# Optimization experiments

Hardware: AMD Instinct MI355X
Metric: run time of the kernel (lower is better)

## Reference

```python
import jax, jax.numpy as jnp
import numpy as np


def setup_inputs() -> dict:
    key = jax.random.key(0)
    k1, k2 = jax.random.split(key)
    N, D, n_bags, per_bag = 8192, 512, 64, 128
    features = jax.random.normal(k1, (N, D), dtype=jnp.float32)
    # sorted bag indicator: 64 bags x 128 instances each
    batch = jnp.repeat(jnp.arange(n_bags, dtype=jnp.int32), per_bag)
    W = jax.random.normal(k2, (D, D), dtype=jnp.float32) * np.float32(1.0 / np.sqrt(D))
    b = jnp.zeros((D,), dtype=jnp.float32)
    return {"features": features, "W": W, "b": b, "batch": batch, "n_topk": 16, "n_bags": n_bags}


def reference(features, W, b, batch, n_topk, n_bags):
    N = features.shape[0]
    # F.normalize(dim=1): x / max(||x||, eps)
    norm = jnp.sqrt(jnp.sum(features * features, axis=1, keepdims=True))
    nf = features / jnp.maximum(norm, 1e-12)
    corr = nf @ nf.T  # [N, N] cosine-similarity map
    same_bag = batch[:, None] == batch[None, :]
    adj = jnp.where(same_bag, corr, 0.0)
    # scatter-zero the (N - n_topk) smallest per row == keep n_topk largest per row
    _, top_idx = jax.lax.top_k(adj, n_topk)  # [N, n_topk]
    keep = jnp.zeros((N, N), dtype=bool).at[jnp.arange(N)[:, None], top_idx].set(True)
    adj = jnp.where(keep, adj, 0.0)
    # dense_to_sparse()[0] keeps only indices -> unit edge weights for GCNConv.
    # GCNConv (gcn_norm, add_self_loops=True): A_hat = binarized adjacency with diag forced to 1.
    eye = jnp.eye(N, dtype=bool)
    A = jnp.where(eye, 1.0, (adj != 0).astype(features.dtype))  # [N, N]
    deg = jnp.sum(A, axis=0)  # degree scattered on target (col) index in PyG
    dis = jax.lax.rsqrt(deg)  # deg >= 1 thanks to self loops
    xw = features @ W  # [N, D]
    # out[col] = d[col]^-1/2 * sum_row A[row,col] * d[row]^-1/2 * xw[row]
    gcn_out = dis[:, None] * (A.T @ (dis[:, None] * xw)) + b
    # one-hot^T @ features == per-bag segment sum
    agg = jax.ops.segment_sum(gcn_out, batch, num_segments=n_bags)  # [n_bags, D]
    return agg, adj
```

## Files before the change

### kernel.cpp

```cpp
#include <hip/hip_runtime.h>
#include <hip/hip_bf16.h>

#define N 8192
#define D 512
#define NBAGS 64
#define PER_BAG 128
#define TOPK 16

typedef float vfloat4 __attribute__((ext_vector_type(4)));

#define WS_INVN   0
#define WS_KIDX   32768
#define WS_KCNT   557056
#define WS_DEG    589824
#define WS_FW     622592

__global__ void norm_kernel(const float* __restrict__ feat,
                            float* __restrict__ invn,
                            int* __restrict__ deg) {
    int t = threadIdx.x;
    if (blockIdx.x < 32) deg[blockIdx.x * 256 + t] = 0;
    int lane = t & 63, w = t >> 6;
    int r = blockIdx.x * 4 + w;
    const float4* fr = (const float4*)(feat + (size_t)r * D);
    float4 a = fr[lane];
    float4 bq = fr[lane + 64];
    float ss = a.x * a.x + a.y * a.y + a.z * a.z + a.w * a.w
             + bq.x * bq.x + bq.y * bq.y + bq.z * bq.z + bq.w * bq.w;
    #pragma unroll
    for (int off = 32; off > 0; off >>= 1) ss += __shfl_down(ss, off);
    if (lane == 0) invn[r] = 1.0f / fmaxf(sqrtf(ss), 1e-12f);
}

__global__ __launch_bounds__(256, 4) void simtopk_kernel(
        const float* __restrict__ feat,
        const float* __restrict__ invn,
        float* __restrict__ adjOut,
        int* __restrict__ keptIdx,
        int* __restrict__ keptCnt,
        int* __restrict__ deg) {
    int rg = blockIdx.x;
    int bag = blockIdx.y;
    int t = threadIdx.x;
    __shared__ float colT[32][132];
    __shared__ float rowT[32][12];
    int bagBase = bag * PER_BAG;
    int rowBase = bagBase + rg * 8;
    int tx = t & 31;
    int ty = t >> 5;
    float4 acc = make_float4(0.f, 0.f, 0.f, 0.f);

    int kk = t & 31;
    int sub = t >> 5;
    int winHalf = bag >> 5;
    int jw = (bag & 31) >> 3;
    int winLo = (bag & 31) * 32, winHi = winLo + 32;
    vfloat4 zf4 = {0.f, 0.f, 0.f, 0.f};

    for (int it = 0; it < 16; ++it) {
        int k0 = it * 32;
        __syncthreads();
        #pragma unroll
        for (int c0 = 0; c0 < 16; ++c0) {
            int c = sub * 16 + c0;
            colT[kk][c] = feat[(size_t)(bagBase + c) * D + k0 + kk];
        }
        rowT[kk][sub] = feat[(size_t)(rowBase + sub) * D + k0 + kk];
        __syncthreads();
        {
            int zr = it >> 1, half = it & 1;
            vfloat4* rowp = (vfloat4*)(adjOut + (size_t)(rowBase + zr) * N)
                            + half * 1024;
            bool hasWin = (half == winHalf);
            #pragma unroll
            for (int j = 0; j < 4; ++j) {
                int f = t + 256 * j;
                if (hasWin && j == jw) {
                    if (f < winLo || f >= winHi)
                        __builtin_nontemporal_store(zf4, &rowp[f]);
                } else {
                    __builtin_nontemporal_store(zf4, &rowp[f]);
                }
            }
        }
        #pragma unroll
        for (int k = 0; k < 32; ++k) {
            float4 cv = *(const float4*)&colT[k][4 * tx];
            float rv = rowT[k][ty];
            acc.x += rv * cv.x; acc.y += rv * cv.y;
            acc.z += rv * cv.z; acc.w += rv * cv.w;
        }
    }
    float ic0 = invn[bagBase + 4 * tx];
    float ic1 = invn[bagBase + 4 * tx + 1];
    float ic2 = invn[bagBase + 4 * tx + 2];
    float ic3 = invn[bagBase + 4 * tx + 3];
    float ir = invn[rowBase + ty];
    acc.x *= ir * ic0; acc.y *= ir * ic1;
    acc.z *= ir * ic2; acc.w *= ir * ic3;

    {
        int r = rowBase + ty;
        float o0 = acc.x, o1 = acc.y, o2 = acc.z, o3 = acc.w;
        float w0 = o0, w1 = o1, w2 = o2, w3 = o3;
        int pm = 0, cnt = 0;
        #pragma unroll 1
        for (int itk = 0; itk < TOPK; ++itk) {
            float bv = w0; int bj = 0;
            if (w1 > bv) { bv = w1; bj = 1; }
            if (w2 > bv) { bv = w2; bj = 2; }
            if (w3 > bv) { bv = w3; bj = 3; }
            int bi = 4 * tx + bj;
            #pragma unroll
            for (int s = 1; s < 32; s <<= 1) {
                float ov = __shfl_xor(bv, s);
                int oi = __shfl_xor(bi, s);
                if (ov > bv || (ov == bv && oi < bi)) { bv = ov; bi = oi; }
            }
            if (bv <= 0.0f) break;
            if (tx == 0) keptIdx[(size_t)r * TOPK + cnt] = bi;
            cnt++;
            if ((bi >> 2) == tx) {
                pm |= 1 << (bi & 3);
                int q = bi & 3;
                if (q == 0) w0 = -1e30f;
                else if (q == 1) w1 = -1e30f;
                else if (q == 2) w2 = -1e30f;
                else w3 = -1e30f;
            }
        }
        if (tx == 0) keptCnt[r] = cnt;
        float4 ov4 = make_float4((pm & 1) ? o0 : 0.0f,
                                 (pm & 2) ? o1 : 0.0f,
                                 (pm & 4) ? o2 : 0.0f,
                                 (pm & 8) ? o3 : 0.0f);
        *(float4*)(adjOut + (size_t)r * N + bagBase + 4 * tx) = ov4;
        if (pm & 1) atomicAdd(&deg[bagBase + 4 * tx], 1);
        if (pm & 2) atomicAdd(&deg[bagBase + 4 * tx + 1], 1);
        if (pm & 4) atomicAdd(&deg[bagBase + 4 * tx + 2], 1);
        if (pm & 8) atomicAdd(&deg[bagBase + 4 * tx + 3], 1);
        int selfCol = rg * 8 + ty;
        if (tx == (selfCol >> 2) && !((pm >> (selfCol & 3)) & 1))
            atomicAdd(&deg[bagBase + selfCol], 1);
    }
}

__global__ void wfw_kernel(const float* __restrict__ feat,
                           const int* __restrict__ keptIdx,
                           const int* __restrict__ keptCnt,
                           const int* __restrict__ deg,
                           float* __restrict__ FW) {
    int bag = blockIdx.x;
    int chunk = blockIdx.y;
    int t = threadIdx.x;
    __shared__ float wsh[PER_BAG];
    int bagBase = bag * PER_BAG;
    {
        int r = bagBase + t;
        int cnt = keptCnt[r];
        float sum = 0.0f;
        bool selfin = false;
        for (int k = 0; k < cnt; ++k) {
            int c = keptIdx[(size_t)r * TOPK + k];
            if (c == t) selfin = true;
            sum += rsqrtf((float)deg[bagBase + c]);
        }
        float disr = rsqrtf((float)deg[r]);
        if (!selfin) sum += disr;
        wsh[t] = disr * sum;
    }
    __syncthreads();
    int d = chunk * 128 + t;
    float acc = 0.0f;
    #pragma unroll 8
    for (int r = 0; r < PER_BAG; ++r)
        acc += wsh[r] * feat[(size_t)(bagBase + r) * D + d];
    FW[bag * D + d] = acc;
}

__global__ void agg_kernel(const float* __restrict__ FW,
                           const float* __restrict__ Wm,
                           const float* __restrict__ b,
                           float* __restrict__ aggOut) {
    int bag = blockIdx.x;
    int chunk = blockIdx.y;
    int t = threadIdx.x;
    __shared__ float fws[D];
    fws[t] = FW[bag * D + t];
    fws[256 + t] = FW[bag * D + 256 + t];
    __syncthreads();
    int d = chunk * 256 + t;
    float acc = 0.0f;
    #pragma unroll 8
    for (int k = 0; k < D; ++k)
        acc += fws[k] * Wm[(size_t)k * D + d];
    aggOut[bag * D + d] = acc + 128.0f * b[d];
}

extern "C" void kernel_launch(void* const* d_in, const int* in_sizes, int n_in,
                              void* d_out, int out_size, void* d_ws, size_t ws_size,
                              hipStream_t stream) {
    const float* feat = (const float*)d_in[0];
    const float* Wm   = (const float*)d_in[1];
    const float* b    = (const float*)d_in[2];

    char* ws = (char*)d_ws;
    float* invn   = (float*)(ws + WS_INVN);
    int* keptIdx  = (int*)(ws + WS_KIDX);
    int* keptCnt  = (int*)(ws + WS_KCNT);
    int* deg      = (int*)(ws + WS_DEG);
    float* FW     = (float*)(ws + WS_FW);

    float* aggOut = (float*)d_out;
    float* adjOut = (float*)d_out + NBAGS * D;

    norm_kernel<<<N / 4, 256, 0, stream>>>(feat, invn, deg);
    simtopk_kernel<<<dim3(16, NBAGS), 256, 0, stream>>>(feat, invn, adjOut,
                                                        keptIdx, keptCnt, deg);
    wfw_kernel<<<dim3(NBAGS, 4), PER_BAG, 0, stream>>>(feat, keptIdx, keptCnt,
                                                       deg, FW);
    agg_kernel<<<dim3(NBAGS, 2), 256, 0, stream>>>(FW, Wm, b, aggOut);
}
```

Measured before the change: 344.3 us.

## Move adjacency zero-fill from simtopk kernel into norm kernel

```diff
diff --git a/kernel.cpp b/kernel.cpp
--- a/kernel.cpp
+++ b/kernel.cpp
@@ -15,13 +15,15 @@
 #define WS_DEG    589824
 #define WS_FW     622592
 
-__global__ void norm_kernel(const float* __restrict__ feat,
-                            float* __restrict__ invn,
-                            int* __restrict__ deg) {
-    int t = threadIdx.x;
-    if (blockIdx.x < 32) deg[blockIdx.x * 256 + t] = 0;
+__global__ void norm_fill_kernel(const float* __restrict__ feat,
+                                 float* __restrict__ invn,
+                                 int* __restrict__ deg,
+                                 float* __restrict__ adjOut) {
+    int t = threadIdx.x;
+    int b = blockIdx.x;
+    if (b < 32) deg[b * 256 + t] = 0;
     int lane = t & 63, w = t >> 6;
-    int r = blockIdx.x * 4 + w;
+    int r = b * 4 + w;
     const float4* fr = (const float4*)(feat + (size_t)r * D);
     float4 a = fr[lane];
     float4 bq = fr[lane + 64];
@@ -30,6 +32,11 @@
     #pragma unroll
     for (int off = 32; off > 0; off >>= 1) ss += __shfl_down(ss, off);
     if (lane == 0) invn[r] = 1.0f / fmaxf(sqrtf(ss), 1e-12f);
+    vfloat4 z = {0.f, 0.f, 0.f, 0.f};
+    vfloat4* base = (vfloat4*)(adjOut + (size_t)b * 4 * N);
+    #pragma unroll
+    for (int j = 0; j < 32; ++j)
+        __builtin_nontemporal_store(z, &base[t + 256 * j]);
 }
 
 __global__ __launch_bounds__(256, 4) void simtopk_kernel(
@@ -52,10 +59,6 @@
 
     int kk = t & 31;
     int sub = t >> 5;
-    int winHalf = bag >> 5;
-    int jw = (bag & 31) >> 3;
-    int winLo = (bag & 31) * 32, winHi = winLo + 32;
-    vfloat4 zf4 = {0.f, 0.f, 0.f, 0.f};
 
     for (int it = 0; it < 16; ++it) {
         int k0 = it * 32;
@@ -67,22 +70,6 @@
         }
         rowT[kk][sub] = feat[(size_t)(rowBase + sub) * D + k0 + kk];
         __syncthreads();
-        {
-            int zr = it >> 1, half = it & 1;
-            vfloat4* rowp = (vfloat4*)(adjOut + (size_t)(rowBase + zr) * N)
-                            + half * 1024;
-            bool hasWin = (half == winHalf);
-            #pragma unroll
-            for (int j = 0; j < 4; ++j) {
-                int f = t + 256 * j;
-                if (hasWin && j == jw) {
-                    if (f < winLo || f >= winHi)
-                        __builtin_nontemporal_store(zf4, &rowp[f]);
-                } else {
-                    __builtin_nontemporal_store(zf4, &rowp[f]);
-                }
-            }
-        }
         #pragma unroll
         for (int k = 0; k < 32; ++k) {
             float4 cv = *(const float4*)&colT[k][4 * tx];
@@ -214,7 +201,7 @@
     float* aggOut = (float*)d_out;
     float* adjOut = (float*)d_out + NBAGS * D;
 
-    norm_kernel<<<N / 4, 256, 0, stream>>>(feat, invn, deg);
+    norm_fill_kernel<<<N / 4, 256, 0, stream>>>(feat, invn, deg, adjOut);
     simtopk_kernel<<<dim3(16, NBAGS), 256, 0, stream>>>(feat, invn, adjOut,
                                                         keptIdx, keptCnt, deg);
     wfw_kernel<<<dim3(NBAGS, 4), PER_BAG, 0, stream>>>(feat, keptIdx, keptCnt,
```

New measurement: 387.9 us. 1.13x slower.

## Fuse norm into simtopk, replace global degree atomics, merge wfw and agg kernels

Applied to the files above, without the earlier changes.

```diff
diff --git a/kernel.cpp b/kernel.cpp
--- a/kernel.cpp
+++ b/kernel.cpp
@@ -9,41 +9,23 @@
 
 typedef float vfloat4 __attribute__((ext_vector_type(4)));
 
-#define WS_INVN   0
-#define WS_KIDX   32768
-#define WS_KCNT   557056
-#define WS_DEG    589824
-#define WS_FW     622592
-
-__global__ void norm_kernel(const float* __restrict__ feat,
-                            float* __restrict__ invn,
-                            int* __restrict__ deg) {
-    int t = threadIdx.x;
-    if (blockIdx.x < 32) deg[blockIdx.x * 256 + t] = 0;
-    int lane = t & 63, w = t >> 6;
-    int r = blockIdx.x * 4 + w;
-    const float4* fr = (const float4*)(feat + (size_t)r * D);
-    float4 a = fr[lane];
-    float4 bq = fr[lane + 64];
-    float ss = a.x * a.x + a.y * a.y + a.z * a.z + a.w * a.w
-             + bq.x * bq.x + bq.y * bq.y + bq.z * bq.z + bq.w * bq.w;
-    #pragma unroll
-    for (int off = 32; off > 0; off >>= 1) ss += __shfl_down(ss, off);
-    if (lane == 0) invn[r] = 1.0f / fmaxf(sqrtf(ss), 1e-12f);
-}
+#define WS_KIDX   0
+#define WS_KCNT   524288
+#define WS_CNT    557056
 
 __global__ __launch_bounds__(256, 4) void simtopk_kernel(
         const float* __restrict__ feat,
-        const float* __restrict__ invn,
         float* __restrict__ adjOut,
         int* __restrict__ keptIdx,
         int* __restrict__ keptCnt,
-        int* __restrict__ deg) {
+        unsigned char* __restrict__ cntOut) {
     int rg = blockIdx.x;
     int bag = blockIdx.y;
     int t = threadIdx.x;
     __shared__ float colT[32][132];
     __shared__ float rowT[32][12];
+    __shared__ float invnS[PER_BAG];
+    __shared__ int cntS[PER_BAG];
     int bagBase = bag * PER_BAG;
     int rowBase = bagBase + rg * 8;
     int tx = t & 31;
@@ -57,13 +39,19 @@
     int winLo = (bag & 31) * 32, winHi = winLo + 32;
     vfloat4 zf4 = {0.f, 0.f, 0.f, 0.f};
 
+    float ssq[16];
+    #pragma unroll
+    for (int c0 = 0; c0 < 16; ++c0) ssq[c0] = 0.0f;
+
     for (int it = 0; it < 16; ++it) {
         int k0 = it * 32;
         __syncthreads();
         #pragma unroll
         for (int c0 = 0; c0 < 16; ++c0) {
             int c = sub * 16 + c0;
-            colT[kk][c] = feat[(size_t)(bagBase + c) * D + k0 + kk];
+            float v = feat[(size_t)(bagBase + c) * D + k0 + kk];
+            colT[kk][c] = v;
+            ssq[c0] += v * v;
         }
         rowT[kk][sub] = feat[(size_t)(rowBase + sub) * D + k0 + kk];
         __syncthreads();
@@ -91,13 +79,21 @@
             acc.z += rv * cv.z; acc.w += rv * cv.w;
         }
     }
-    float ic0 = invn[bagBase + 4 * tx];
-    float ic1 = invn[bagBase + 4 * tx + 1];
-    float ic2 = invn[bagBase + 4 * tx + 2];
-    float ic3 = invn[bagBase + 4 * tx + 3];
-    float ir = invn[rowBase + ty];
-    acc.x *= ir * ic0; acc.y *= ir * ic1;
-    acc.z *= ir * ic2; acc.w *= ir * ic3;
+
+    #pragma unroll
+    for (int c0 = 0; c0 < 16; ++c0) {
+        float s = ssq[c0];
+        #pragma unroll
+        for (int m = 1; m < 32; m <<= 1) s += __shfl_xor(s, m);
+        if (kk == c0) invnS[sub * 16 + c0] = 1.0f / fmaxf(sqrtf(s), 1e-12f);
+    }
+    if (t < PER_BAG) cntS[t] = 0;
+    __syncthreads();
+
+    float4 icv = *(const float4*)&invnS[4 * tx];
+    float ir = invnS[rg * 8 + ty];
+    acc.x *= ir * icv.x; acc.y *= ir * icv.y;
+    acc.z *= ir * icv.z; acc.w *= ir * icv.w;
 
     {
         int r = rowBase + ty;
@@ -135,66 +131,72 @@
                                  (pm & 4) ? o2 : 0.0f,
                                  (pm & 8) ? o3 : 0.0f);
         *(float4*)(adjOut + (size_t)r * N + bagBase + 4 * tx) = ov4;
-        if (pm & 1) atomicAdd(&deg[bagBase + 4 * tx], 1);
-        if (pm & 2) atomicAdd(&deg[bagBase + 4 * tx + 1], 1);
-        if (pm & 4) atomicAdd(&deg[bagBase + 4 * tx + 2], 1);
-        if (pm & 8) atomicAdd(&deg[bagBase + 4 * tx + 3], 1);
+        if (pm & 1) atomicAdd(&cntS[4 * tx], 1);
+        if (pm & 2) atomicAdd(&cntS[4 * tx + 1], 1);
+        if (pm & 4) atomicAdd(&cntS[4 * tx + 2], 1);
+        if (pm & 8) atomicAdd(&cntS[4 * tx + 3], 1);
         int selfCol = rg * 8 + ty;
         if (tx == (selfCol >> 2) && !((pm >> (selfCol & 3)) & 1))
-            atomicAdd(&deg[bagBase + selfCol], 1);
-    }
+            atomicAdd(&cntS[selfCol], 1);
+    }
+    __syncthreads();
+    if (t < PER_BAG)
+        cntOut[(bag * 16 + rg) * PER_BAG + t] = (unsigned char)cntS[t];
 }
 
-__global__ void wfw_kernel(const float* __restrict__ feat,
-                           const int* __restrict__ keptIdx,
-                           const int* __restrict__ keptCnt,
-                           const int* __restrict__ deg,
-                           float* __restrict__ FW) {
+__global__ void wfwagg_kernel(const float* __restrict__ feat,
+                              const int* __restrict__ keptIdx,
+                              const int* __restrict__ keptCnt,
+                              const unsigned char* __restrict__ cnt,
+                              const float* __restrict__ Wm,
+                              const float* __restrict__ b,
+                              float* __restrict__ aggOut) {
     int bag = blockIdx.x;
     int chunk = blockIdx.y;
     int t = threadIdx.x;
+    __shared__ float dis[PER_BAG];
     __shared__ float wsh[PER_BAG];
+    __shared__ float fw[D];
     int bagBase = bag * PER_BAG;
-    {
+    if (t < PER_BAG) {
+        int dsum = 0;
+        #pragma unroll
+        for (int rgi = 0; rgi < 16; ++rgi)
+            dsum += cnt[(bag * 16 + rgi) * PER_BAG + t];
+        dis[t] = rsqrtf((float)dsum);
+    }
+    __syncthreads();
+    if (t < PER_BAG) {
         int r = bagBase + t;
-        int cnt = keptCnt[r];
+        int c2 = keptCnt[r];
         float sum = 0.0f;
         bool selfin = false;
-        for (int k = 0; k < cnt; ++k) {
+        for (int k = 0; k < c2; ++k) {
             int c = keptIdx[(size_t)r * TOPK + k];
             if (c == t) selfin = true;
-            sum += rsqrtf((float)deg[bagBase + c]);
-        }
-        float disr = rsqrtf((float)deg[r]);
+            sum += dis[c];
+        }
+        float disr = dis[t];
         if (!selfin) sum += disr;
         wsh[t] = disr * sum;
     }
     __syncthreads();
-    int d = chunk * 128 + t;
-    float acc = 0.0f;
-    #pragma unroll 8
-    for (int r = 0; r < PER_BAG; ++r)
-        acc += wsh[r] * feat[(size_t)(bagBase + r) * D + d];
-    FW[bag * D + d] = acc;
-}
-
-__global__ void agg_kernel(const float* __restrict__ FW,
-                           const float* __restrict__ Wm,
-                           const float* __restrict__ b,
-                           float* __restrict__ aggOut) {
-    int bag = blockIdx.x;
-    int chunk = blockIdx.y;
-    int t = threadIdx.x;
-    __shared__ float fws[D];
-    fws[t] = FW[bag * D + t];
-    fws[256 + t] = FW[bag * D + 256 + t];
+    #pragma unroll
+    for (int dd = 0; dd < 2; ++dd) {
+        int d = t + 256 * dd;
+        float a = 0.0f;
+        #pragma unroll 8
+        for (int r = 0; r < PER_BAG; ++r)
+            a += wsh[r] * feat[(size_t)(bagBase + r) * D + d];
+        fw[d] = a;
+    }
     __syncthreads();
     int d = chunk * 256 + t;
-    float acc = 0.0f;
+    float a = 0.0f;
     #pragma unroll 8
     for (int k = 0; k < D; ++k)
-        acc += fws[k] * Wm[(size_t)k * D + d];
-    aggOut[bag * D + d] = acc + 128.0f * b[d];
+        a += fw[k] * Wm[(size_t)k * D + d];
+    aggOut[bag * D + d] = a + 128.0f * b[d];
 }
 
 extern "C" void kernel_launch(void* const* d_in, const int* in_sizes, int n_in,
@@ -205,19 +207,16 @@
     const float* b    = (const float*)d_in[2];
 
     char* ws = (char*)d_ws;
-    float* invn   = (float*)(ws + WS_INVN);
-    int* keptIdx  = (int*)(ws + WS_KIDX);
-    int* keptCnt  = (int*)(ws + WS_KCNT);
-    int* deg      = (int*)(ws + WS_DEG);
-    float* FW     = (float*)(ws + WS_FW);
+    int* keptIdx           = (int*)(ws + WS_KIDX);
+    int* keptCnt           = (int*)(ws + WS_KCNT);
+    unsigned char* cntBuf  = (unsigned char*)(ws + WS_CNT);
 
     float* aggOut = (float*)d_out;
     float* adjOut = (float*)d_out + NBAGS * D;
 
-    norm_kernel<<<N / 4, 256, 0, stream>>>(feat, invn, deg);
-    simtopk_kernel<<<dim3(16, NBAGS), 256, 0, stream>>>(feat, invn, adjOut,
-                                                        keptIdx, keptCnt, deg);
-    wfw_kernel<<<dim3(NBAGS, 4), PER_BAG, 0, stream>>>(feat, keptIdx, keptCnt,
-                                                       deg, FW);
-    agg_kernel<<<dim3(NBAGS, 2), 256, 0, stream>>>(FW, Wm, b, aggOut);
+    simtopk_kernel<<<dim3(16, NBAGS), 256, 0, stream>>>(feat, adjOut,
+                                                        keptIdx, keptCnt,
+                                                        cntBuf);
+    wfwagg_kernel<<<dim3(NBAGS, 2), 256, 0, stream>>>(feat, keptIdx, keptCnt,
+                                                      cntBuf, Wm, b, aggOut);
 }
```

Measured after the change: 366.9 us. 6.6% more time.
